# Performance work log

Hardware: AMD Instinct MI355X
Metric: run time of the kernel (lower is better)

Reference implementation:

```python
import jax, jax.numpy as jnp
import numpy as np

E4M3 = jnp.float8_e4m3fn  # HPU e4m3 (max 240) approximated by e4m3fn grid
E5M2 = jnp.float8_e5m2


def fp8_quant_dequant(x, scale, dt):
    # cast_to_fp8(x, scale) followed by inline dequant (1/scale) inside fp8_gemm_v2
    return (x * scale).astype(dt).astype(jnp.float32) / scale


def setup_inputs() -> dict:
    key = jax.random.key(0)
    k1, k2 = jax.random.split(key)
    A, B, C, OUT = 4, 2048, 2048, 8192
    return {
        "input": jax.random.normal(k1, (A, B, C), jnp.float32),
        "weight": jax.random.normal(k2, (OUT, C), jnp.float32) * 0.02,
        "input_scale_e4m3": jnp.ones((), jnp.float32),
        "weight_scale_e4m3": jnp.ones((), jnp.float32),
        "input_scale_e5m2": jnp.ones((), jnp.float32),
        "weight_scale_e5m2": jnp.ones((), jnp.float32),
        "grad_scale_e5m2": jnp.ones((), jnp.float32),
    }


def reference(input, weight, input_scale_e4m3, weight_scale_e4m3,
              input_scale_e5m2, weight_scale_e5m2, grad_scale_e5m2):
    A, B, C = input.shape
    x2d = input.reshape(A * B, C)
    # forward path uses the e4m3 copies from cast_to_fp8_hybrid
    x_q = fp8_quant_dequant(x2d, input_scale_e4m3, E4M3)      # [A*B, C]
    w_q = fp8_quant_dequant(weight, weight_scale_e4m3, E4M3)  # [OUT, C]
    out = x_q @ w_q.T                                          # [A*B, OUT]
    return out.reshape(A, B, -1)
```

## Files before the change

kernel.cpp:

```cpp
#include <hip/hip_runtime.h>

typedef float floatx16 __attribute__((ext_vector_type(16)));
typedef int   intx4    __attribute__((ext_vector_type(4)));
typedef int   intx8    __attribute__((ext_vector_type(8)));

#define GEMM_M 8192
#define GEMM_N 8192
#define GEMM_K 2048

__global__ __launch_bounds__(256) void quant_e4m3(const float* __restrict__ x,
                                                  const float* __restrict__ scale,
                                                  int* __restrict__ q)
{
    const float s = scale[0];
    const int base = blockIdx.x * 1024 + threadIdx.x;
    const float4* __restrict__ x4 = (const float4*)x;
#pragma unroll
    for (int j = 0; j < 4; ++j) {
        float4 v = x4[base + j * 256];
        int p;
        p = __builtin_amdgcn_cvt_pk_fp8_f32(v.x * s, v.y * s, 0, false);
        p = __builtin_amdgcn_cvt_pk_fp8_f32(v.z * s, v.w * s, p, true);
        q[base + j * 256] = p;
    }
}

__global__ __launch_bounds__(256, 2) void gemm_fp8_mx(
    const unsigned char* __restrict__ Aq,
    const unsigned char* __restrict__ Bq,
    float* __restrict__ C,
    const float* __restrict__ sa,
    const float* __restrict__ sb)
{
    __shared__ __align__(16) unsigned char sA[128 * 64];
    __shared__ __align__(16) unsigned char sB[256 * 64];

    const int tid  = threadIdx.x;
    const int lane = tid & 63;
    const int wave = tid >> 6;
    const int bn   = blockIdx.x;
    const int bm   = blockIdx.y;

    const int rseg = lane >> 2;
    const int cswz = (((lane & 3) ^ ((lane >> 3) & 3)) << 4);

    const unsigned char* gA[2];
    unsigned char*       lA[2];
#pragma unroll
    for (int t = 0; t < 2; ++t) {
        const int s = wave * 2 + t;
        gA[t] = Aq + (size_t)(bm * 128 + s * 16 + rseg) * GEMM_K + cswz;
        lA[t] = &sA[s * 1024 + lane * 16];
    }
    const unsigned char* gB[4];
    unsigned char*       lB[4];
#pragma unroll
    for (int t = 0; t < 4; ++t) {
        const int s = wave * 4 + t;
        gB[t] = Bq + (size_t)(bn * 256 + s * 16 + rseg) * GEMM_K + cswz;
        lB[t] = &sB[s * 1024 + lane * 16];
    }

    const int mloc = lane & 31;
    const int h    = lane >> 5;
    const int swz  = (mloc >> 1) & 3;
    const int wm   = wave >> 1, wn = wave & 1;

    unsigned alo[2], ahi[2];
#pragma unroll
    for (int t = 0; t < 2; ++t) {
        const unsigned row = (unsigned)(wm * 64 + t * 32 + mloc) << 6;
        alo[t] = row + (((2 * h + 0) ^ swz) << 4);
        ahi[t] = row + (((2 * h + 1) ^ swz) << 4);
    }
    unsigned blo[4], bhi[4];
#pragma unroll
    for (int t = 0; t < 4; ++t) {
        const unsigned row = (unsigned)(wn * 128 + t * 32 + mloc) << 6;
        blo[t] = row + (((2 * h + 0) ^ swz) << 4);
        bhi[t] = row + (((2 * h + 1) ^ swz) << 4);
    }

    floatx16 acc[2][4];
#pragma unroll
    for (int i = 0; i < 2; ++i)
#pragma unroll
        for (int j = 0; j < 4; ++j)
            acc[i][j] = (floatx16)(0.0f);

    for (int kt = 0; kt < GEMM_K / 64; ++kt) {
        const int kb = kt * 64;
#pragma unroll
        for (int t = 0; t < 2; ++t)
            __builtin_amdgcn_global_load_lds(
                (const __attribute__((address_space(1))) void*)(gA[t] + kb),
                (__attribute__((address_space(3))) void*)lA[t], 16, 0, 0);
#pragma unroll
        for (int t = 0; t < 4; ++t)
            __builtin_amdgcn_global_load_lds(
                (const __attribute__((address_space(1))) void*)(gB[t] + kb),
                (__attribute__((address_space(3))) void*)lB[t], 16, 0, 0);
        __syncthreads();

        intx8 a[2], b[4];
#pragma unroll
        for (int t = 0; t < 2; ++t) {
            intx4 lo = *(const intx4*)&sA[alo[t]];
            intx4 hi = *(const intx4*)&sA[ahi[t]];
            a[t] = __builtin_shufflevector(lo, hi, 0, 1, 2, 3, 4, 5, 6, 7);
        }
#pragma unroll
        for (int t = 0; t < 4; ++t) {
            intx4 lo = *(const intx4*)&sB[blo[t]];
            intx4 hi = *(const intx4*)&sB[bhi[t]];
            b[t] = __builtin_shufflevector(lo, hi, 0, 1, 2, 3, 4, 5, 6, 7);
        }

#pragma unroll
        for (int i = 0; i < 2; ++i)
#pragma unroll
            for (int j = 0; j < 4; ++j)
                acc[i][j] = __builtin_amdgcn_mfma_scale_f32_32x32x64_f8f6f4(
                    a[i], b[j], acc[i][j],
                    0, 0,
                    0, 0x7f7f7f7f,
                    0, 0x7f7f7f7f);

        __syncthreads();
    }

    const float inv = 1.0f / (sa[0] * sb[0]);
#pragma unroll
    for (int ti = 0; ti < 2; ++ti) {
        const int row0 = bm * 128 + wm * 64 + ti * 32 + 4 * h;
#pragma unroll
        for (int tj = 0; tj < 4; ++tj) {
            const int col = bn * 256 + wn * 128 + tj * 32 + mloc;
#pragma unroll
            for (int reg = 0; reg < 16; ++reg) {
                const int row = row0 + (reg & 3) + 8 * (reg >> 2);
                C[(size_t)row * GEMM_N + col] = acc[ti][tj][reg] * inv;
            }
        }
    }
}

extern "C" void kernel_launch(void* const* d_in, const int* in_sizes, int n_in,
                              void* d_out, int out_size, void* d_ws, size_t ws_size,
                              hipStream_t stream) {
    const float* x    = (const float*)d_in[0];
    const float* w    = (const float*)d_in[1];
    const float* s_in = (const float*)d_in[2];
    const float* s_w  = (const float*)d_in[3];
    float* out = (float*)d_out;

    unsigned char* qx = (unsigned char*)d_ws;
    unsigned char* qw = qx + (size_t)GEMM_M * GEMM_K;

    quant_e4m3<<<in_sizes[0] / 4096, 256, 0, stream>>>(x, s_in, (int*)qx);
    quant_e4m3<<<in_sizes[1] / 4096, 256, 0, stream>>>(w, s_w, (int*)qw);

    dim3 grid(GEMM_N / 256, GEMM_M / 128);
    gemm_fp8_mx<<<grid, 256, 0, stream>>>(qx, qw, out, s_in, s_w);
}
```

Before: 485.0 us.

## Restructure FP8 GEMM into 256x256 tiles with a 4-stage LDS pipeline

Raises the block tile from 128x256 to 256x256 with 512 threads (8 waves) and adds a 4-deep ring of LDS buffers in 128KB of dynamic shared memory. Global-to-LDS loads for stage k+3 are issued while stage k computes, and explicit vmcnt waits with a single barrier per step replace the two full syncthreads. It also remaps block ids into a grouped order for L2 reuse and raises wave priority around the MFMA bursts. The aim is to hide memory latency and cut barrier stalls, at the cost of more LDS per block, which limits how many blocks fit per CU, and of reliance on hand-written waitcnt counts.

```diff
diff --git a/kernel.cpp b/kernel.cpp
--- a/kernel.cpp
+++ b/kernel.cpp
@@ -7,6 +7,7 @@
 #define GEMM_M 8192
 #define GEMM_N 8192
 #define GEMM_K 2048
+#define NT     32
 
 __global__ __launch_bounds__(256) void quant_e4m3(const float* __restrict__ x,
                                                   const float* __restrict__ scale,
@@ -25,117 +26,121 @@
     }
 }
 
-__global__ __launch_bounds__(256, 2) void gemm_fp8_mx(
+#define GLDS(gp, lp) __builtin_amdgcn_global_load_lds( \
+    (const __attribute__((address_space(1))) void*)(gp), \
+    (__attribute__((address_space(3))) void*)(lp), 16, 0, 0)
+
+__global__ __launch_bounds__(512, 2) void gemm_fp8_mx(
     const unsigned char* __restrict__ Aq,
     const unsigned char* __restrict__ Bq,
     float* __restrict__ C,
     const float* __restrict__ sa,
     const float* __restrict__ sb)
 {
-    __shared__ __align__(16) unsigned char sA[128 * 64];
-    __shared__ __align__(16) unsigned char sB[256 * 64];
+    extern __shared__ __align__(16) unsigned char lds[];
+    unsigned char* ldsA = lds;
+    unsigned char* ldsB = lds + 65536;
 
     const int tid  = threadIdx.x;
     const int lane = tid & 63;
     const int wave = tid >> 6;
-    const int bn   = blockIdx.x;
-    const int bm   = blockIdx.y;
+    const int wm   = wave >> 2;
+    const int wn   = wave & 3;
 
-    const int rseg = lane >> 2;
-    const int cswz = (((lane & 3) ^ ((lane >> 3) & 3)) << 4);
+    const int bid = blockIdx.x;
+    const int nb  = (bid & 7) * 128 + (bid >> 3);
+    const int bm  = nb >> 5;
+    const int bn  = nb & 31;
 
-    const unsigned char* gA[2];
-    unsigned char*       lA[2];
-#pragma unroll
-    for (int t = 0; t < 2; ++t) {
-        const int s = wave * 2 + t;
-        gA[t] = Aq + (size_t)(bm * 128 + s * 16 + rseg) * GEMM_K + cswz;
-        lA[t] = &sA[s * 1024 + lane * 16];
-    }
-    const unsigned char* gB[4];
-    unsigned char*       lB[4];
-#pragma unroll
-    for (int t = 0; t < 4; ++t) {
-        const int s = wave * 4 + t;
-        gB[t] = Bq + (size_t)(bn * 256 + s * 16 + rseg) * GEMM_K + cswz;
-        lB[t] = &sB[s * 1024 + lane * 16];
-    }
+    const int srow   = tid >> 2;
+    const int schunk = ((tid & 3) ^ ((tid >> 3) & 3)) << 4;
+    const unsigned char* gA0 = Aq + (size_t)(bm * 256 +       srow) * GEMM_K + schunk;
+    const unsigned char* gA1 = Aq + (size_t)(bm * 256 + 128 + srow) * GEMM_K + schunk;
+    const unsigned char* gB0 = Bq + (size_t)(bn * 256 +       srow) * GEMM_K + schunk;
+    const unsigned char* gB1 = Bq + (size_t)(bn * 256 + 128 + srow) * GEMM_K + schunk;
+    const int l0 = tid * 16;
 
     const int mloc = lane & 31;
     const int h    = lane >> 5;
     const int swz  = (mloc >> 1) & 3;
-    const int wm   = wave >> 1, wn = wave & 1;
+    const int aoff_lo = (wm * 128 + mloc) * 64 + (((2 * h)     ^ swz) << 4);
+    const int aoff_hi = (wm * 128 + mloc) * 64 + (((2 * h + 1) ^ swz) << 4);
+    const int boff_lo = (wn * 64  + mloc) * 64 + (((2 * h)     ^ swz) << 4);
+    const int boff_hi = (wn * 64  + mloc) * 64 + (((2 * h + 1) ^ swz) << 4);
 
-    unsigned alo[2], ahi[2];
+    floatx16 acc[4][2];
 #pragma unroll
-    for (int t = 0; t < 2; ++t) {
-        const unsigned row = (unsigned)(wm * 64 + t * 32 + mloc) << 6;
-        alo[t] = row + (((2 * h + 0) ^ swz) << 4);
-        ahi[t] = row + (((2 * h + 1) ^ swz) << 4);
-    }
-    unsigned blo[4], bhi[4];
+    for (int i = 0; i < 4; ++i)
 #pragma unroll
-    for (int t = 0; t < 4; ++t) {
-        const unsigned row = (unsigned)(wn * 128 + t * 32 + mloc) << 6;
-        blo[t] = row + (((2 * h + 0) ^ swz) << 4);
-        bhi[t] = row + (((2 * h + 1) ^ swz) << 4);
-    }
-
-    floatx16 acc[2][4];
-#pragma unroll
-    for (int i = 0; i < 2; ++i)
-#pragma unroll
-        for (int j = 0; j < 4; ++j)
+        for (int j = 0; j < 2; ++j)
             acc[i][j] = (floatx16)(0.0f);
 
-    for (int kt = 0; kt < GEMM_K / 64; ++kt) {
-        const int kb = kt * 64;
-#pragma unroll
-        for (int t = 0; t < 2; ++t)
-            __builtin_amdgcn_global_load_lds(
-                (const __attribute__((address_space(1))) void*)(gA[t] + kb),
-                (__attribute__((address_space(3))) void*)lA[t], 16, 0, 0);
-#pragma unroll
-        for (int t = 0; t < 4; ++t)
-            __builtin_amdgcn_global_load_lds(
-                (const __attribute__((address_space(1))) void*)(gB[t] + kb),
-                (__attribute__((address_space(3))) void*)lB[t], 16, 0, 0);
-        __syncthreads();
+#define STAGE(KT) do { \
+    const int _b = (KT) & 3; \
+    const size_t _ko = (size_t)(KT) * 64; \
+    GLDS(gA0 + _ko, ldsA + _b * 16384 +        l0); \
+    GLDS(gA1 + _ko, ldsA + _b * 16384 + 8192 + l0); \
+    GLDS(gB0 + _ko, ldsB + _b * 16384 +        l0); \
+    GLDS(gB1 + _ko, ldsB + _b * 16384 + 8192 + l0); \
+} while (0)
 
-        intx8 a[2], b[4];
-#pragma unroll
-        for (int t = 0; t < 2; ++t) {
-            intx4 lo = *(const intx4*)&sA[alo[t]];
-            intx4 hi = *(const intx4*)&sA[ahi[t]];
-            a[t] = __builtin_shufflevector(lo, hi, 0, 1, 2, 3, 4, 5, 6, 7);
-        }
-#pragma unroll
-        for (int t = 0; t < 4; ++t) {
-            intx4 lo = *(const intx4*)&sB[blo[t]];
-            intx4 hi = *(const intx4*)&sB[bhi[t]];
-            b[t] = __builtin_shufflevector(lo, hi, 0, 1, 2, 3, 4, 5, 6, 7);
-        }
+#define KSTEP(KT, STAGE_STMT) do { \
+    const unsigned char* _bA = ldsA + ((KT) & 3) * 16384; \
+    const unsigned char* _bB = ldsB + ((KT) & 3) * 16384; \
+    intx8 _a[4], _bf[2]; \
+    _Pragma("unroll") \
+    for (int _t = 0; _t < 4; ++_t) { \
+        intx4 lo = *(const intx4*)(_bA + aoff_lo + _t * 2048); \
+        intx4 hi = *(const intx4*)(_bA + aoff_hi + _t * 2048); \
+        _a[_t] = __builtin_shufflevector(lo, hi, 0, 1, 2, 3, 4, 5, 6, 7); \
+    } \
+    _Pragma("unroll") \
+    for (int _t = 0; _t < 2; ++_t) { \
+        intx4 lo = *(const intx4*)(_bB + boff_lo + _t * 2048); \
+        intx4 hi = *(const intx4*)(_bB + boff_hi + _t * 2048); \
+        _bf[_t] = __builtin_shufflevector(lo, hi, 0, 1, 2, 3, 4, 5, 6, 7); \
+    } \
+    STAGE_STMT; \
+    __builtin_amdgcn_s_setprio(1); \
+    _Pragma("unroll") \
+    for (int _i = 0; _i < 4; ++_i) \
+    _Pragma("unroll") \
+    for (int _j = 0; _j < 2; ++_j) \
+        acc[_i][_j] = __builtin_amdgcn_mfma_scale_f32_32x32x64_f8f6f4( \
+            _a[_i], _bf[_j], acc[_i][_j], \
+            0, 0, 0, 0x7f7f7f7f, 0, 0x7f7f7f7f); \
+    __builtin_amdgcn_s_setprio(0); \
+} while (0)
 
-#pragma unroll
-        for (int i = 0; i < 2; ++i)
-#pragma unroll
-            for (int j = 0; j < 4; ++j)
-                acc[i][j] = __builtin_amdgcn_mfma_scale_f32_32x32x64_f8f6f4(
-                    a[i], b[j], acc[i][j],
-                    0, 0,
-                    0, 0x7f7f7f7f,
-                    0, 0x7f7f7f7f);
+#define BARRIER() do { asm volatile("" ::: "memory"); \
+    __builtin_amdgcn_s_barrier(); \
+    asm volatile("" ::: "memory"); } while (0)
 
-        __syncthreads();
+    STAGE(0); STAGE(1); STAGE(2);
+    asm volatile("s_waitcnt vmcnt(8)" ::: "memory");
+    BARRIER();
+
+#pragma unroll 1
+    for (int kt = 0; kt <= NT - 4; ++kt) {
+        KSTEP(kt, STAGE(kt + 3));
+        asm volatile("s_waitcnt vmcnt(8)" ::: "memory");
+        BARRIER();
     }
+    KSTEP(NT - 3, (void)0);
+    asm volatile("s_waitcnt vmcnt(4)" ::: "memory");
+    BARRIER();
+    KSTEP(NT - 2, (void)0);
+    asm volatile("s_waitcnt vmcnt(0)" ::: "memory");
+    BARRIER();
+    KSTEP(NT - 1, (void)0);
 
     const float inv = 1.0f / (sa[0] * sb[0]);
 #pragma unroll
-    for (int ti = 0; ti < 2; ++ti) {
-        const int row0 = bm * 128 + wm * 64 + ti * 32 + 4 * h;
+    for (int ti = 0; ti < 4; ++ti) {
+        const int row0 = bm * 256 + wm * 128 + ti * 32 + 4 * h;
 #pragma unroll
-        for (int tj = 0; tj < 4; ++tj) {
-            const int col = bn * 256 + wn * 128 + tj * 32 + mloc;
+        for (int tj = 0; tj < 2; ++tj) {
+            const int col = bn * 256 + wn * 64 + tj * 32 + mloc;
 #pragma unroll
             for (int reg = 0; reg < 16; ++reg) {
                 const int row = row0 + (reg & 3) + 8 * (reg >> 2);
@@ -160,6 +165,11 @@
     quant_e4m3<<<in_sizes[0] / 4096, 256, 0, stream>>>(x, s_in, (int*)qx);
     quant_e4m3<<<in_sizes[1] / 4096, 256, 0, stream>>>(w, s_w, (int*)qw);
 
-    dim3 grid(GEMM_N / 256, GEMM_M / 128);
-    gemm_fp8_mx<<<grid, 256, 0, stream>>>(qx, qw, out, s_in, s_w);
+    static int attr_done = 0;
+    if (!attr_done) {
+        hipFuncSetAttribute((const void*)gemm_fp8_mx,
+                            hipFuncAttributeMaxDynamicSharedMemorySize, 131072);
+        attr_done = 1;
+    }
+    gemm_fp8_mx<<<dim3(1024), dim3(512), 131072, stream>>>(qx, qw, out, s_in, s_w);
 }
```

Result: no change. 487.4 us (+0.5%).
